# Optimization experiments

Hardware: AMD Instinct MI355X
Metric: run time of the kernel (lower is better)

The kernel has to match this reference:

```python
import jax, jax.numpy as jnp
import numpy as np

B0, B1 = 4096, 4096  # batch dims; 16.7M fp16 values


def setup_inputs() -> dict:
    key = jax.random.key(0)
    # binary pulse representation of FP16: [S, E4..E0, M9..M0], MSB first
    bits = jax.random.randint(key, (B0, B1, 16), 0, 2).astype(jnp.float32)
    return {"fp16_pulse": bits}


def _rne_shift(x, k):
    """Round-to-nearest-even of (x >> k); k may be a per-element int array."""
    keep = jnp.right_shift(x, k)
    rbit = jnp.right_shift(x, k - 1) & 1                      # guard/round bit
    low_mask = jnp.left_shift(jnp.int32(1), k - 1) - 1
    sticky = ((x & low_mask) > 0).astype(jnp.int32)           # OR of all lower bits
    round_up = rbit & (sticky | (keep & 1))                   # RNE: R & (S | L)
    return keep + round_up


def _convert(bits):
    """FP16 -> FP8 E4M3 via the same bit-level semantics as the SNN gate chain:
    exp_fp8 = exp_fp16 - 8, 3-bit mantissa with RNE rounding, subnormal outputs
    for fp16 exp fields 5..8, underflow->0 for exp<5, saturate for exp>22."""
    b = bits.astype(jnp.int32)
    s = b[..., 0]
    e = jnp.einsum('...k,k->...', b[..., 1:6],
                   jnp.array([16, 8, 4, 2, 1], jnp.int32))     # 5-bit exponent field
    m = jnp.einsum('...k,k->...', b[..., 6:16],
                   jnp.array([512, 256, 128, 64, 32, 16, 8, 4, 2, 1], jnp.int32))

    # --- normal path (fp16 exp field 9..22): keep m9..m7, RNE on the 7 dropped bits
    mant_r = _rne_shift(m, jnp.full_like(m, 7))                # 0..8 (carry possible)
    norm_e = (e - 8) + (mant_r >> 3)                           # exponent bump on carry
    norm_m = mant_r & 7                                        # 111+1 -> 000 automatically

    # --- subnormal / boundary path (fp16 exp field 5..8):
    # FP8 subnormal M = RNE((1024 + m) >> (16 - e)); M==8 promotes to normal E=1,M=0
    k = jnp.clip(16 - e, 8, 11)
    m_sub = _rne_shift(1024 + m, k)                            # 0..8
    sub_e = m_sub >> 3                                         # 1 iff rounded up to normal
    sub_m = jnp.where(m_sub >= 8, 0, m_sub)

    # --- select per the comparators in the module
    is_ovf = e > 22           # overflow_cmp vs const 22
    is_unf = e < 5            # underflow_cmp vs const 5
    is_sub = (e >= 5) & (e <= 8)  # exp_cmp_5/6/7 + is_lt_8 boundary
    out_e = jnp.where(is_ovf, 15, jnp.where(is_unf, 0, jnp.where(is_sub, sub_e, norm_e)))
    out_m = jnp.where(is_ovf, 6,  jnp.where(is_unf, 0, jnp.where(is_sub, sub_m, norm_m)))

    eb = jnp.stack([(out_e >> 3) & 1, (out_e >> 2) & 1, (out_e >> 1) & 1, out_e & 1], axis=-1)
    mb = jnp.stack([(out_m >> 2) & 1, (out_m >> 1) & 1, out_m & 1], axis=-1)
    return jnp.concatenate([s[..., None], eb, mb], axis=-1).astype(bits.dtype)


def reference(fp16_pulse):
    return _convert(fp16_pulse)
```

## Files before the change

kernel.cpp:

```cpp
#include <hip/hip_runtime.h>


typedef unsigned int u32;
typedef u32 u32x4 __attribute__((ext_vector_type(4)));

__global__ __launch_bounds__(256) void fp16_to_fp8_pulse_kernel(
    const u32x4* __restrict__ in,
    u32x4* __restrict__ out,
    int n_items)
{
    int i = blockIdx.x * blockDim.x + threadIdx.x;
    if (i >= n_items) return;

    const u32x4 v0 = __builtin_nontemporal_load(&in[4 * i + 0]);
    const u32x4 v1 = __builtin_nontemporal_load(&in[4 * i + 1]);
    const u32x4 v2 = __builtin_nontemporal_load(&in[4 * i + 2]);
    const u32x4 v3 = __builtin_nontemporal_load(&in[4 * i + 3]);

#define BIT(w) (((w) >> 23) & 1u)
    const u32 s = BIT(v0.x);
    const u32 e = (BIT(v0.y) << 4) | (BIT(v0.z) << 3) | (BIT(v0.w) << 2) |
                  (BIT(v1.x) << 1) |  BIT(v1.y);
    const u32 m = (BIT(v1.z) << 9) | (BIT(v1.w) << 8) | (BIT(v2.x) << 7) |
                  (BIT(v2.y) << 6) | (BIT(v2.z) << 5) | (BIT(v2.w) << 4) |
                  (BIT(v3.x) << 3) | (BIT(v3.y) << 2) | (BIT(v3.z) << 1) |
                   BIT(v3.w);
#undef BIT

    const u32 keep_n   = m >> 7;
    const u32 rbit_n   = (m >> 6) & 1u;
    const u32 sticky_n = (m & 63u) ? 1u : 0u;
    const u32 mant_r   = keep_n + (rbit_n & (sticky_n | (keep_n & 1u)));
    const u32 norm_e   = (e - 8u) + (mant_r >> 3);
    const u32 norm_m   = mant_r & 7u;

    u32 k = 16u - e;
    k = k < 8u ? 8u : (k > 11u ? 11u : k);
    const u32 x        = 1024u + m;
    const u32 keep_s   = x >> k;
    const u32 rbit_s   = (x >> (k - 1u)) & 1u;
    const u32 sticky_s = (x & ((1u << (k - 1u)) - 1u)) ? 1u : 0u;
    const u32 m_sub    = keep_s + (rbit_s & (sticky_s | (keep_s & 1u)));
    const u32 sub_e    = m_sub >> 3;
    const u32 sub_m    = (m_sub >= 8u) ? 0u : m_sub;

    const u32 out_e = (e > 22u) ? 15u : (e < 5u) ? 0u : (e <= 8u) ? sub_e : norm_e;
    const u32 out_m = (e > 22u) ? 6u  : (e < 5u) ? 0u : (e <= 8u) ? sub_m : norm_m;

#define PULSE(b) ((0u - (b)) & 0x3F800000u)
    u32x4 o0, o1;
    o0.x = PULSE(s);
    o0.y = PULSE((out_e >> 3) & 1u);
    o0.z = PULSE((out_e >> 2) & 1u);
    o0.w = PULSE((out_e >> 1) & 1u);
    o1.x = PULSE(out_e & 1u);
    o1.y = PULSE((out_m >> 2) & 1u);
    o1.z = PULSE((out_m >> 1) & 1u);
    o1.w = PULSE(out_m & 1u);
#undef PULSE

    __builtin_nontemporal_store(o0, &out[2 * i + 0]);
    __builtin_nontemporal_store(o1, &out[2 * i + 1]);
}

extern "C" void kernel_launch(void* const* d_in, const int* in_sizes, int n_in,
                              void* d_out, int out_size, void* d_ws, size_t ws_size,
                              hipStream_t stream) {
    const u32x4* in = (const u32x4*)d_in[0];
    u32x4* out = (u32x4*)d_out;

    const int n_items = in_sizes[0] / 16;
    const int block = 256;
    const int grid = (n_items + block - 1) / block;

    fp16_to_fp8_pulse_kernel<<<grid, block, 0, stream>>>(in, out, n_items);
}
```

Measured before the change: 1.558 ms.

## Split each element across four lanes with coalesced loads and shuffle reassembly

Four adjacent threads now share one FP16 element. Each thread loads one 16-byte chunk, so consecutive lanes read consecutive addresses. The 4-bit nibbles are combined into the 16-bit word with two xor shuffles, every lane redundantly computes the FP8 byte, and each lane writes 8 bytes of output. This replaces the strided 64-byte-per-thread loads and 32-byte stores with fully coalesced access, at the cost of four times the threads, shuffle overhead, and dropping the nontemporal hints.

```diff
diff --git a/kernel.cpp b/kernel.cpp
--- a/kernel.cpp
+++ b/kernel.cpp
@@ -3,29 +3,31 @@
 
 typedef unsigned int u32;
 typedef u32 u32x4 __attribute__((ext_vector_type(4)));
+typedef u32 u32x2 __attribute__((ext_vector_type(2)));
 
 __global__ __launch_bounds__(256) void fp16_to_fp8_pulse_kernel(
     const u32x4* __restrict__ in,
-    u32x4* __restrict__ out,
-    int n_items)
+    u32x2* __restrict__ out,
+    int n4)
 {
-    int i = blockIdx.x * blockDim.x + threadIdx.x;
-    if (i >= n_items) return;
+    const int g = blockIdx.x * blockDim.x + threadIdx.x;
+    if (g >= n4) return;
 
-    const u32x4 v0 = __builtin_nontemporal_load(&in[4 * i + 0]);
-    const u32x4 v1 = __builtin_nontemporal_load(&in[4 * i + 1]);
-    const u32x4 v2 = __builtin_nontemporal_load(&in[4 * i + 2]);
-    const u32x4 v3 = __builtin_nontemporal_load(&in[4 * i + 3]);
+    const u32x4 v = in[g];
+    const u32 p = (u32)(threadIdx.x & 3);
 
 #define BIT(w) (((w) >> 23) & 1u)
-    const u32 s = BIT(v0.x);
-    const u32 e = (BIT(v0.y) << 4) | (BIT(v0.z) << 3) | (BIT(v0.w) << 2) |
-                  (BIT(v1.x) << 1) |  BIT(v1.y);
-    const u32 m = (BIT(v1.z) << 9) | (BIT(v1.w) << 8) | (BIT(v2.x) << 7) |
-                  (BIT(v2.y) << 6) | (BIT(v2.z) << 5) | (BIT(v2.w) << 4) |
-                  (BIT(v3.x) << 3) | (BIT(v3.y) << 2) | (BIT(v3.z) << 1) |
-                   BIT(v3.w);
+    const u32 nib = (BIT(v.x) << 3) | (BIT(v.y) << 2) | (BIT(v.z) << 1) | BIT(v.w);
 #undef BIT
+
+    const u32 o1   = (u32)__shfl_xor((int)nib, 1);
+    const u32 pair = (p & 1u) ? ((o1 << 4) | nib) : ((nib << 4) | o1);
+    const u32 o2   = (u32)__shfl_xor((int)pair, 2);
+    const u32 word = (p & 2u) ? ((o2 << 8) | pair) : ((pair << 8) | o2);
+
+    const u32 s = word >> 15;
+    const u32 e = (word >> 10) & 31u;
+    const u32 m = word & 1023u;
 
     const u32 keep_n   = m >> 7;
     const u32 rbit_n   = (m >> 6) & 1u;
@@ -47,31 +49,26 @@
     const u32 out_e = (e > 22u) ? 15u : (e < 5u) ? 0u : (e <= 8u) ? sub_e : norm_e;
     const u32 out_m = (e > 22u) ? 6u  : (e < 5u) ? 0u : (e <= 8u) ? sub_m : norm_m;
 
-#define PULSE(b) ((0u - (b)) & 0x3F800000u)
-    u32x4 o0, o1;
-    o0.x = PULSE(s);
-    o0.y = PULSE((out_e >> 3) & 1u);
-    o0.z = PULSE((out_e >> 2) & 1u);
-    o0.w = PULSE((out_e >> 1) & 1u);
-    o1.x = PULSE(out_e & 1u);
-    o1.y = PULSE((out_m >> 2) & 1u);
-    o1.z = PULSE((out_m >> 1) & 1u);
-    o1.w = PULSE(out_m & 1u);
-#undef PULSE
+    const u32 obyte = (s << 7) | (out_e << 3) | out_m;
 
-    __builtin_nontemporal_store(o0, &out[2 * i + 0]);
-    __builtin_nontemporal_store(o1, &out[2 * i + 1]);
+    const u32 hi = (obyte >> (7u - 2u * p)) & 1u;
+    const u32 lo = (obyte >> (6u - 2u * p)) & 1u;
+
+    u32x2 o;
+    o.x = (0u - hi) & 0x3F800000u;
+    o.y = (0u - lo) & 0x3F800000u;
+    out[g] = o;
 }
 
 extern "C" void kernel_launch(void* const* d_in, const int* in_sizes, int n_in,
                               void* d_out, int out_size, void* d_ws, size_t ws_size,
                               hipStream_t stream) {
     const u32x4* in = (const u32x4*)d_in[0];
-    u32x4* out = (u32x4*)d_out;
+    u32x2* out = (u32x2*)d_out;
 
-    const int n_items = in_sizes[0] / 16;
+    const int n4 = in_sizes[0] / 4;
     const int block = 256;
-    const int grid = (n_items + block - 1) / block;
+    const int grid = (n4 + block - 1) / block;
 
-    fp16_to_fp8_pulse_kernel<<<grid, block, 0, stream>>>(in, out, n_items);
+    fp16_to_fp8_pulse_kernel<<<grid, block, 0, stream>>>(in, out, n4);
 }
```

Result: faster. 1.437 ms (-7.7%).
